# Kernel optimization log

Measured on AMD Instinct MI355X. Metric: run time of the kernel, lower is better.

Reference implementation:

```python
import jax, jax.numpy as jnp
import numpy as np

B, N, D = 256, 128, 512
NUM_TYPES, NUM_STATS = 6, 8
W_TYPE, W_STATS, W_CORR = 1.0, 1.0, 0.5
LN_EPS = 1e-5


def setup_inputs() -> dict:
    key = jax.random.key(0)
    ks = jax.random.split(key, 20)
    s = 1.0 / np.sqrt(D)
    inp = {
        "column_embeddings": jax.random.normal(ks[0], (B, N, D), jnp.float32),
        "masked_columns": jax.random.bernoulli(ks[1], 0.15, (B, N)),
        "type_targets": jax.random.randint(ks[2], (N,), 0, NUM_TYPES),
        "column_statistics": jax.random.normal(ks[3], (B, N, NUM_STATS), jnp.float32),
        "column_correlations": jnp.tanh(jax.random.normal(ks[4], (B, N, N), jnp.float32)),
        # type head: Linear(D,D) -> GELU -> LayerNorm -> Linear(D,NUM_TYPES)
        "t_W1": jax.random.normal(ks[5], (D, D), jnp.float32) * s,
        "t_b1": jnp.zeros((D,), jnp.float32),
        "t_g": jnp.ones((D,), jnp.float32),
        "t_beta": jnp.zeros((D,), jnp.float32),
        "t_W2": jax.random.normal(ks[6], (D, NUM_TYPES), jnp.float32) * s,
        "t_b2": jnp.zeros((NUM_TYPES,), jnp.float32),
        # stats head
        "s_W1": jax.random.normal(ks[7], (D, D), jnp.float32) * s,
        "s_b1": jnp.zeros((D,), jnp.float32),
        "s_g": jnp.ones((D,), jnp.float32),
        "s_beta": jnp.zeros((D,), jnp.float32),
        "s_W2": jax.random.normal(ks[8], (D, NUM_STATS), jnp.float32) * s,
        "s_b2": jnp.zeros((NUM_STATS,), jnp.float32),
        # bilinear correlation: x_i^T W x_j + b
        "c_W": jax.random.normal(ks[9], (D, D), jnp.float32) * s,
        "c_b": jnp.zeros((), jnp.float32),
    }
    return inp


def _mlp_head(x, W1, b1, g, beta, W2, b2):
    h = jax.nn.gelu(x @ W1 + b1, approximate=False)
    mu = h.mean(-1, keepdims=True)
    var = ((h - mu) ** 2).mean(-1, keepdims=True)
    h = (h - mu) * jax.lax.rsqrt(var + LN_EPS) * g + beta
    return h @ W2 + b2


def _forward(column_embeddings, masked_columns, type_targets,
             column_statistics, column_correlations,
             t_W1, t_b1, t_g, t_beta, t_W2, t_b2,
             s_W1, s_b1, s_g, s_beta, s_W2, s_b2,
             c_W, c_b):
    e = column_embeddings  # [B,N,D]
    type_logits = _mlp_head(e, t_W1, t_b1, t_g, t_beta, t_W2, t_b2)   # [B,N,T]
    stats_preds = _mlp_head(e, s_W1, s_b1, s_g, s_beta, s_W2, s_b2)   # [B,N,S]

    # batched bilinear correlation: tanh(e_i W e_j + b), diag forced to 1
    u = jnp.einsum('bnd,de->bne', e, c_W)            # [B,N,D]
    corr = jnp.tanh(jnp.einsum('bne,bme->bnm', u, e) + c_b)  # [B,N,N]
    eye = jnp.eye(e.shape[1], dtype=corr.dtype)
    corr = corr * (1.0 - eye) + eye

    m = masked_columns.astype(jnp.float32)           # [B,N]
    n_masked = jnp.maximum(m.sum(), 1.0)

    # type loss: masked-mean cross entropy; targets broadcast over batch
    logp = jax.nn.log_softmax(type_logits, axis=-1)
    tgt = jnp.broadcast_to(type_targets[None, :], m.shape)
    ce = -jnp.take_along_axis(logp, tgt[..., None], axis=-1)[..., 0]  # [B,N]
    type_loss = (ce * m).sum() / n_masked

    # stats loss: masked-mean MSE over [B,N,S]
    se = (stats_preds - column_statistics) ** 2
    stats_loss = (se * m[..., None]).sum() / (n_masked * se.shape[-1])

    # correlation loss: mask_expanded = m_i | m_j
    me = jnp.maximum(m[:, :, None], m[:, None, :])   # [B,N,N]
    n_me = jnp.maximum(me.sum(), 1.0)
    ce2 = (corr - column_correlations) ** 2
    correlation_loss = (ce2 * me).sum() / n_me

    total = W_TYPE * type_loss + W_STATS * stats_loss + W_CORR * correlation_loss
    return total


def reference(column_embeddings, masked_columns, type_targets,
              column_statistics, column_correlations,
              t_W1, t_b1, t_g, t_beta, t_W2, t_b2,
              s_W1, s_b1, s_g, s_beta, s_W2, s_b2,
              c_W, c_b):
    return _forward(column_embeddings, masked_columns, type_targets,
                    column_statistics, column_correlations,
                    t_W1, t_b1, t_g, t_beta, t_W2, t_b2,
                    s_W1, s_b1, s_g, s_beta, s_W2, s_b2,
                    c_W, c_b)
```

## Files before the change

### kernel.cpp

```cpp
#include <hip/hip_runtime.h>
#include <math.h>

#define Bx 256
#define Nx 128
#define Dx 512
#define NTYPES 6
#define NSTATS 8
#define LN_EPS 1e-5f
#define CAP 8192

typedef __attribute__((ext_vector_type(8))) short frag8;
typedef __attribute__((ext_vector_type(4))) float f32x4;

__device__ __forceinline__ unsigned short f2bf(float f) {
    unsigned u = __float_as_uint(f);
    u += 0x7fff + ((u >> 16) & 1);
    return (unsigned short)(u >> 16);
}
__device__ __forceinline__ float bf2f(unsigned short s) {
    return __uint_as_float((unsigned)s << 16);
}

#define ASYNC16(g, l) __builtin_amdgcn_global_load_lds(                      \
    (const __attribute__((address_space(1))) void*)(g),                      \
    (__attribute__((address_space(3))) void*)(l), 16, 0, 0)

#define VWAIT(NIMM)                                                          \
    asm volatile("s_waitcnt vmcnt(" #NIMM ")" ::: "memory");                 \
    __builtin_amdgcn_sched_barrier(0);
#define BARX __builtin_amdgcn_s_barrier();

#define EB_OFF    0ULL
#define HC_OFF    33554432ULL
#define WT_OFF    67108864ULL
#define WTC_OFF   68157440ULL
#define WC_OFF    68681728ULL
#define LIST_OFF  69206016ULL
#define CNTS_OFF  69238784ULL
#define BASES_OFF 69239808ULL
#define CNTP_OFF  69240832ULL
#define ACC_OFF   69240848ULL
#define DONE_OFF  69240864ULL

__global__ __launch_bounds__(256) void k_prep(
    const float* __restrict__ e, const float* __restrict__ W0,
    const float* __restrict__ W1, const float* __restrict__ W2,
    unsigned short* __restrict__ Eb, unsigned short* __restrict__ Tcmb,
    unsigned short* __restrict__ Tc, unsigned short* __restrict__ Wc,
    const int* __restrict__ m, int* __restrict__ list,
    int* __restrict__ cnts, int* __restrict__ bases, int* cntp) {
    const int bid = blockIdx.x;
    const int t = threadIdx.x;
    if (bid < 256) {
        const int b = bid;
        const int r = b * Nx + t;
        int v = 0;
        if (t < 128) v = (m[r] != 0) ? 1 : 0;
        const unsigned long long bal = __ballot(v);
        const int wid = t >> 6, lane = t & 63;
        __shared__ int wcnt[2];
        __shared__ int base;
        if (lane == 0 && wid < 2) wcnt[wid] = __popcll(bal);
        __syncthreads();
        const int cnt = wcnt[0] + wcnt[1];
        if (t == 0) {
            base = atomicAdd(cntp, cnt);
            cnts[b] = cnt;
            bases[b] = base;
        }
        __syncthreads();
        if (t < 128 && v) {
            const int rank = __popcll(bal & ((1ULL << lane) - 1)) +
                             (wid ? wcnt[0] : 0);
            const int p = base + rank;
            if (p < CAP) list[p] = r;
        }
        return;
    }
    if (bid < 448) {
        const int lin = bid - 256;
        const int mid = lin >> 6;
        const int tl  = lin & 63;
        const int ti = tl >> 3, tj = tl & 7;
        const float* W = (mid == 0) ? W0 : (mid == 1) ? W1 : W2;
        unsigned short* T = (mid == 2) ? Tc : (Tcmb + mid * 262144);
        __shared__ float sh[64][65];
        const int c = t & 63;
        const int r4 = t >> 6;
#pragma unroll
        for (int rr = 0; rr < 16; ++rr) {
            const int row = rr * 4 + r4;
            sh[row][c] = W[(size_t)(ti * 64 + row) * Dx + tj * 64 + c];
        }
        __syncthreads();
#pragma unroll
        for (int rr = 0; rr < 16; ++rr) {
            const int col2 = rr * 4 + r4;
            T[(size_t)(tj * 64 + col2) * Dx + ti * 64 + c] = f2bf(sh[c][col2]);
        }
        return;
    }
    if (bid < 512) {
        const int base = (bid - 448) * 4096 + t * 16;
        const float4* src = (const float4*)(W2 + base);
        unsigned short o[16];
#pragma unroll
        for (int q = 0; q < 4; ++q) {
            const float4 v = src[q];
            o[q * 4 + 0] = f2bf(v.x); o[q * 4 + 1] = f2bf(v.y);
            o[q * 4 + 2] = f2bf(v.z); o[q * 4 + 3] = f2bf(v.w);
        }
        *(uint4*)(Wc + base) = *(const uint4*)(o);
        *(uint4*)(Wc + base + 8) = *(const uint4*)(o + 8);
        return;
    }
    const int r = (bid - 512) * 4 + (t >> 6);
    const int lane = t & 63;
    const float4* src = (const float4*)(e + (size_t)r * Dx);
    const float4 a = src[lane * 2];
    const float4 b = src[lane * 2 + 1];
    unsigned short u[8] = {f2bf(a.x), f2bf(a.y), f2bf(a.z), f2bf(a.w),
                           f2bf(b.x), f2bf(b.y), f2bf(b.z), f2bf(b.w)};
    ((uint4*)(Eb + (size_t)r * Dx))[lane] = *(const uint4*)u;
}

__global__ __launch_bounds__(512) void k_gemms(
    const unsigned short* __restrict__ Eb,
    const unsigned short* __restrict__ Wtcmb,
    const unsigned short* __restrict__ Wtc,
    const unsigned short* __restrict__ Wc,
    const float* __restrict__ bias0, const float* __restrict__ bias1,
    unsigned short* __restrict__ Hc,
    const int* __restrict__ list, const int* __restrict__ cntp) {
    __shared__ unsigned short As[2 * 4096];
    __shared__ unsigned short Bs[2 * 8192];
    const int bid = blockIdx.x;
    const int t = threadIdx.x;
    const int cnt = min(*cntp, CAP);
    const int rt = ((bid >> 6) << 3) | (bid & 7);
    const int row0 = rt << 7;
    if (row0 >= cnt) return;
    const int ct = (bid >> 3) & 7;
    const int col0 = ct << 8;
    const unsigned short* Bbase =
        (ct < 4) ? (Wtcmb + (size_t)ct * 256 * Dx)
      : (ct < 6) ? (Wtc + (size_t)(ct - 4) * 256 * Dx)
                 : (Wc + (size_t)(ct - 6) * 256 * Dx);
    const int kq = (t & 3) ^ ((t >> 3) & 3);
    const int ra = list[min(row0 + (t >> 2), cnt - 1)];
    const unsigned short* pA = Eb + (size_t)ra * Dx + kq * 8;
    const unsigned short* pB0 = Bbase + (size_t)(t >> 2) * Dx + kq * 8;
    const unsigned short* pB1 = pB0 + (size_t)128 * Dx;
    const int w = t >> 6, l = t & 63;
    const int wr = (w >> 2) * 64, wcol = (w & 3) * 64;
    const int quad = l >> 4, mr = l & 15;
    const int co = (quad ^ ((mr >> 1) & 3)) * 8;

#define MSTAGE(bf, k0)                                                       \
  { ASYNC16(pA + (k0), As + (bf) * 4096 + t * 8);                            \
    ASYNC16(pB0 + (k0), Bs + (bf) * 8192 + t * 8);                           \
    ASYNC16(pB1 + (k0), Bs + (bf) * 8192 + 4096 + t * 8); }

    f32x4 acc[4][4] = {};
    MSTAGE(0, 0);
    int buf = 0;
    for (int k = 0; k < 16; ++k) {
        if (k < 15) { MSTAGE(buf ^ 1, (k + 1) * 32); VWAIT(3); }
        else        { VWAIT(0); }
        BARX;
        frag8 af[4], bfv[4];
#pragma unroll
        for (int i = 0; i < 4; ++i)
            af[i] = *(const frag8*)&As[buf * 4096 + (wr + i * 16 + mr) * 32 + co];
#pragma unroll
        for (int j = 0; j < 4; ++j)
            bfv[j] = *(const frag8*)&Bs[buf * 8192 + (wcol + j * 16 + mr) * 32 + co];
        __builtin_amdgcn_s_setprio(1);
#pragma unroll
        for (int i = 0; i < 4; ++i)
#pragma unroll
            for (int j = 0; j < 4; ++j)
                acc[i][j] = __builtin_amdgcn_mfma_f32_16x16x32_bf16(
                    af[i], bfv[j], acc[i][j], 0, 0, 0);
        __builtin_amdgcn_s_setprio(0);
        if (k < 15) BARX;
        buf ^= 1;
    }
#pragma unroll
    for (int i = 0; i < 4; ++i)
#pragma unroll
        for (int j = 0; j < 4; ++j)
#pragma unroll
            for (int r = 0; r < 4; ++r) {
                const int row = row0 + wr + i * 16 + quad * 4 + r;
                const int col = col0 + wcol + j * 16 + mr;
                float v = acc[i][j][r];
                if (col < 1024) {
                    v += (col < 512) ? bias0[col] : bias1[col - 512];
                    v = 0.5f * v * (1.0f + erff(v * 0.70710678118654752f));
                }
                Hc[(size_t)row * 2048 + col] = f2bf(v);
            }
#undef MSTAGE
}

__global__ __launch_bounds__(256) void k_tail(
    const unsigned short* __restrict__ Eb,
    const float* __restrict__ Ct, const int* __restrict__ m,
    const float* __restrict__ cbp,
    const unsigned short* __restrict__ Hc,
    const float* __restrict__ tg, const float* __restrict__ tbeta,
    const float* __restrict__ tW2, const float* __restrict__ tb2,
    const float* __restrict__ sg, const float* __restrict__ sbeta,
    const float* __restrict__ sW2, const float* __restrict__ sb2,
    const int* __restrict__ list, const int* __restrict__ cnts,
    const int* __restrict__ bases, const int* __restrict__ cntp,
    const int* __restrict__ tgt, const float* __restrict__ stats,
    float* __restrict__ accs, int* __restrict__ done,
    float* __restrict__ out) {
    __shared__ unsigned short Elds[2 * 4096];
    __shared__ unsigned short Ulds[2 * 1024];
    __shared__ unsigned short Vlds[2 * 1024];
    __shared__ float mloc[128];
    __shared__ int lrow[128];
    __shared__ float redf[4][2];
    const int t = threadIdx.x;
    const int w = t >> 6, l = t & 63;
    const int quad = l >> 4, mr = l & 15;

    if (blockIdx.x < 256) {
        const int b = blockIdx.x;
        const int cnt = cnts[b];
        const int cbase = bases[b];
        if (t < 128) {
            mloc[t] = (m[b * Nx + t] != 0) ? 1.0f : 0.0f;
            lrow[t] = (t < cnt) ? (list[cbase + t] & (Nx - 1)) : 0;
        }
        __syncthreads();
        float T1 = 0.0f, T2 = 0.0f, Tov = 0.0f;
        const float cb = cbp[0];
        const float* Ctb = Ct + (size_t)b * Nx * Nx;
        if (cnt > 0) {
            const int kq = (t & 3) ^ ((t >> 3) & 3);
            const size_t rb = (size_t)b * Nx;
            const unsigned short* pE0 = Eb + (rb + (t >> 2)) * Dx + kq * 8;
            const unsigned short* pE1 = Eb + (rb + 64 + (t >> 2)) * Dx + kq * 8;
            const int co = (quad ^ ((mr >> 1) & 3)) * 8;
            const int hw = t >> 7;
            const int t2 = t & 127;

            for (int c0 = 0; c0 < cnt; c0 += 32) {
                const int ntc = min(((cnt - c0) + 15) >> 4, 2);
                const int urow = min(c0 + (t2 >> 2), cnt - 1);
                const unsigned short* pUV = Hc + (size_t)(cbase + urow) * 2048
                                            + (hw ? 1536 : 1024) + kq * 8;
                unsigned short* UVdst = hw ? Vlds : Ulds;

#define TSTAGE(bf, ph)                                                       \
  { ASYNC16(pE0 + (ph) * 32, Elds + (bf) * 4096 + t * 8);                    \
    ASYNC16(pE1 + (ph) * 32, Elds + (bf) * 4096 + 2048 + t * 8);             \
    ASYNC16(pUV + (ph) * 32, UVdst + (bf) * 1024 + t2 * 8); }

                f32x4 ar[2][2] = {};
                f32x4 ac[2][2] = {};
                TSTAGE(0, 0);
                int buf = 0;
                for (int k = 0; k < 16; ++k) {
                    if (k < 15) { TSTAGE(buf ^ 1, k + 1); VWAIT(3); }
                    else        { VWAIT(0); }
                    BARX;
                    frag8 ef[2];
#pragma unroll
                    for (int eidx = 0; eidx < 2; ++eidx)
                        ef[eidx] = *(const frag8*)&Elds[buf * 4096 +
                            (w * 32 + eidx * 16 + mr) * 32 + co];
                    __builtin_amdgcn_s_setprio(1);
#pragma unroll
                    for (int it = 0; it < 2; ++it)
                        if (it < ntc) {
                            const frag8 uf = *(const frag8*)&Ulds[buf * 1024 +
                                (it * 16 + mr) * 32 + co];
                            ar[it][0] = __builtin_amdgcn_mfma_f32_16x16x32_bf16(
                                uf, ef[0], ar[it][0], 0, 0, 0);
                            ar[it][1] = __builtin_amdgcn_mfma_f32_16x16x32_bf16(
                                uf, ef[1], ar[it][1], 0, 0, 0);
                        }
#pragma unroll
                    for (int jt = 0; jt < 2; ++jt)
                        if (jt < ntc) {
                            const frag8 vf = *(const frag8*)&Vlds[buf * 1024 +
                                (jt * 16 + mr) * 32 + co];
                            ac[0][jt] = __builtin_amdgcn_mfma_f32_16x16x32_bf16(
                                ef[0], vf, ac[0][jt], 0, 0, 0);
                            ac[1][jt] = __builtin_amdgcn_mfma_f32_16x16x32_bf16(
                                ef[1], vf, ac[1][jt], 0, 0, 0);
                        }
                    __builtin_amdgcn_s_setprio(0);
                    if (k < 15) BARX;
                    buf ^= 1;
                }
#pragma unroll
                for (int it = 0; it < 2; ++it)
                    if (it < ntc) {
#pragma unroll
                        for (int eidx = 0; eidx < 2; ++eidx) {
                            const int j = w * 32 + eidx * 16 + mr;
#pragma unroll
                            for (int r = 0; r < 4; ++r) {
                                const int pos = c0 + it * 16 + quad * 4 + r;
                                if (pos < cnt) {
                                    const int i = lrow[pos];
                                    const float s = ar[it][eidx][r];
                                    const float c = (i == j) ? 1.0f
                                                             : tanhf(s + cb);
                                    const float d = c - Ctb[i * Nx + j];
                                    T1 += d * d;
                                    Tov += d * d * mloc[j];
                                }
                            }
                        }
                    }
#pragma unroll
                for (int jt = 0; jt < 2; ++jt)
                    if (jt < ntc) {
                        const int pos = c0 + jt * 16 + mr;
                        const int valid = (pos < cnt);
                        const int j = lrow[pos & 127];
#pragma unroll
                        for (int eidx = 0; eidx < 2; ++eidx) {
#pragma unroll
                            for (int r = 0; r < 4; ++r) {
                                if (valid) {
                                    const int i = w * 32 + eidx * 16 +
                                                  quad * 4 + r;
                                    const float s = ac[eidx][jt][r];
                                    const float c = (i == j) ? 1.0f
                                                             : tanhf(s + cb);
                                    const float d = c - Ctb[i * Nx + j];
                                    T2 += d * d;
                                }
                            }
                        }
                    }
#undef TSTAGE
            }
        }
        float lsum = T1 + T2 - Tov;
#pragma unroll
        for (int off = 32; off > 0; off >>= 1) lsum += __shfl_down(lsum, off);
        if (l == 0) redf[w][0] = lsum;
        __syncthreads();
        if (t == 0) {
            atomicAdd(&accs[2], redf[0][0] + redf[1][0] + redf[2][0] + redf[3][0]);
            const float c = (float)cnt;
            atomicAdd(&accs[3], 256.0f * c - c * c);
        }
    } else {
        const int blk = blockIdx.x - 256;
        const int cnt = min(*cntp, CAP);
        float ce_acc = 0.0f, sse_acc = 0.0f;
        for (int idx = blk * 4 + w; idx < cnt; idx += 256 * 4) {
            const int r = list[idx];
            const uint4 ut = ((const uint4*)(Hc + (size_t)idx * 2048))[l];
            const uint4 us = ((const uint4*)(Hc + (size_t)idx * 2048 + 512))[l];
            float a[8], b8[8];
            {
                const unsigned uu[4] = {ut.x, ut.y, ut.z, ut.w};
                const unsigned vv[4] = {us.x, us.y, us.z, us.w};
#pragma unroll
                for (int j = 0; j < 4; ++j) {
                    a[2 * j]      = bf2f((unsigned short)(uu[j] & 0xffff));
                    a[2 * j + 1]  = bf2f((unsigned short)(uu[j] >> 16));
                    b8[2 * j]     = bf2f((unsigned short)(vv[j] & 0xffff));
                    b8[2 * j + 1] = bf2f((unsigned short)(vv[j] >> 16));
                }
            }
            float st = 0, qt = 0, ss = 0, qs = 0;
#pragma unroll
            for (int j = 0; j < 8; ++j) {
                st += a[j]; qt += a[j] * a[j];
                ss += b8[j]; qs += b8[j] * b8[j];
            }
#pragma unroll
            for (int off = 32; off > 0; off >>= 1) {
                st += __shfl_xor(st, off); qt += __shfl_xor(qt, off);
                ss += __shfl_xor(ss, off); qs += __shfl_xor(qs, off);
            }
            const float mt = st * (1.0f / Dx);
            const float rt = rsqrtf(qt * (1.0f / Dx) - mt * mt + LN_EPS);
            const float ms = ss * (1.0f / Dx);
            const float rs = rsqrtf(qs * (1.0f / Dx) - ms * ms + LN_EPS);

            const int c0 = l * 8;
            float tp[6] = {}, sp[8] = {};
#pragma unroll
            for (int j = 0; j < 8; ++j) {
                const int c = c0 + j;
                const float nt2 = (a[j] - mt) * rt * tg[c] + tbeta[c];
#pragma unroll
                for (int k = 0; k < 6; ++k) tp[k] += nt2 * tW2[c * 6 + k];
                const float ns = (b8[j] - ms) * rs * sg[c] + sbeta[c];
#pragma unroll
                for (int k = 0; k < 8; ++k) sp[k] += ns * sW2[c * 8 + k];
            }
#pragma unroll
            for (int k = 0; k < 6; ++k)
#pragma unroll
                for (int off = 32; off > 0; off >>= 1) tp[k] += __shfl_down(tp[k], off);
#pragma unroll
            for (int k = 0; k < 8; ++k)
#pragma unroll
                for (int off = 32; off > 0; off >>= 1) sp[k] += __shfl_down(sp[k], off);

            if (l == 0) {
                float lg[6];
#pragma unroll
                for (int k = 0; k < 6; ++k) lg[k] = tp[k] + tb2[k];
                float mx = lg[0];
#pragma unroll
                for (int k = 1; k < 6; ++k) mx = fmaxf(mx, lg[k]);
                float se = 0.0f;
#pragma unroll
                for (int k = 0; k < 6; ++k) se += expf(lg[k] - mx);
                ce_acc += -(lg[tgt[r & (Nx - 1)]] - mx - logf(se));
                float sse = 0.0f;
#pragma unroll
                for (int k = 0; k < 8; ++k) {
                    const float d = sp[k] + sb2[k] - stats[(size_t)r * NSTATS + k];
                    sse += d * d;
                }
                sse_acc += sse;
            }
        }
        if (l == 0) { redf[w][0] = ce_acc; redf[w][1] = sse_acc; }
        __syncthreads();
        if (t == 0) {
            atomicAdd(&accs[0], redf[0][0] + redf[1][0] + redf[2][0] + redf[3][0]);
            atomicAdd(&accs[1], redf[0][1] + redf[1][1] + redf[2][1] + redf[3][1]);
        }
    }
    __syncthreads();
    if (t == 0) {
        __threadfence();
        const int old = atomicAdd(done, 1);
        if (old == 511) {
            __threadfence();
            const float CE  = atomicAdd(&accs[0], 0.0f);
            const float SSE = atomicAdd(&accs[1], 0.0f);
            const float CO  = atomicAdd(&accs[2], 0.0f);
            const float ME  = atomicAdd(&accs[3], 0.0f);
            const float nm = fmaxf((float)min(*cntp, CAP), 1.0f);
            out[0] = CE / nm + SSE / (nm * (float)NSTATS) +
                     0.5f * CO / fmaxf(ME, 1.0f);
        }
    }
}

extern "C" void kernel_launch(void* const* d_in, const int* in_sizes, int n_in,
                              void* d_out, int out_size, void* d_ws, size_t ws_size,
                              hipStream_t stream) {
    const float* e      = (const float*)d_in[0];
    const int*   mcols  = (const int*)d_in[1];
    const int*   ttgt   = (const int*)d_in[2];
    const float* stats  = (const float*)d_in[3];
    const float* corrT  = (const float*)d_in[4];
    const float* tW1    = (const float*)d_in[5];
    const float* tb1    = (const float*)d_in[6];
    const float* tg     = (const float*)d_in[7];
    const float* tbeta  = (const float*)d_in[8];
    const float* tW2    = (const float*)d_in[9];
    const float* tb2    = (const float*)d_in[10];
    const float* sW1    = (const float*)d_in[11];
    const float* sb1    = (const float*)d_in[12];
    const float* sg     = (const float*)d_in[13];
    const float* sbeta  = (const float*)d_in[14];
    const float* sW2    = (const float*)d_in[15];
    const float* sb2    = (const float*)d_in[16];
    const float* cW     = (const float*)d_in[17];
    const float* cb     = (const float*)d_in[18];
    float* out = (float*)d_out;

    char* ws = (char*)d_ws;
    unsigned short* Eb    = (unsigned short*)(ws + EB_OFF);
    unsigned short* Hc    = (unsigned short*)(ws + HC_OFF);
    unsigned short* Wtcmb = (unsigned short*)(ws + WT_OFF);
    unsigned short* Wtc   = (unsigned short*)(ws + WTC_OFF);
    unsigned short* Wc    = (unsigned short*)(ws + WC_OFF);
    int*   list  = (int*)(ws + LIST_OFF);
    int*   cnts  = (int*)(ws + CNTS_OFF);
    int*   bases = (int*)(ws + BASES_OFF);
    int*   cntp  = (int*)(ws + CNTP_OFF);
    float* accs  = (float*)(ws + ACC_OFF);
    int*   done  = (int*)(ws + DONE_OFF);

    hipMemsetAsync(ws + CNTP_OFF, 0, 48, stream);
    k_prep<<<8704, 256, 0, stream>>>(e, tW1, sW1, cW, Eb, Wtcmb, Wtc, Wc,
                                     mcols, list, cnts, bases, cntp);
    k_gemms<<<512, 512, 0, stream>>>(Eb, Wtcmb, Wtc, Wc, tb1, sb1, Hc,
                                     list, cntp);
    k_tail<<<512, 256, 0, stream>>>(Eb, corrT, mcols, cb, Hc,
                                    tg, tbeta, tW2, tb2, sg, sbeta, sW2, sb2,
                                    list, cnts, bases, cntp, ttgt, stats,
                                    accs, done, out);
}
```

Before: 226.0 us.

## Split correlation tail work into half-batch blocks with triple-buffered async loads

The correlation part of k_tail now launches two blocks per batch, each handling 64 of the 128 columns, so there are 512 correlation blocks instead of 256. That doubles parallelism and halves per-block MFMA and register accumulators. The E/U/V LDS staging moves from a double buffer to a three-stage ring with prefetch two steps ahead, so load latency overlaps with compute. The cost is that each U/V tile is loaded twice (once per half-block), and the mask-count atomic is restricted to one half to avoid double counting.

```diff
diff --git a/kernel.cpp b/kernel.cpp
--- a/kernel.cpp
+++ b/kernel.cpp
@@ -218,9 +218,9 @@
     const int* __restrict__ tgt, const float* __restrict__ stats,
     float* __restrict__ accs, int* __restrict__ done,
     float* __restrict__ out) {
-    __shared__ unsigned short Elds[2 * 4096];
-    __shared__ unsigned short Ulds[2 * 1024];
-    __shared__ unsigned short Vlds[2 * 1024];
+    __shared__ unsigned short Elds[3 * 2048];
+    __shared__ unsigned short Ulds[3 * 1024];
+    __shared__ unsigned short Vlds[3 * 1024];
     __shared__ float mloc[128];
     __shared__ int lrow[128];
     __shared__ float redf[4][2];
@@ -228,8 +228,9 @@
     const int w = t >> 6, l = t & 63;
     const int quad = l >> 4, mr = l & 15;
 
-    if (blockIdx.x < 256) {
-        const int b = blockIdx.x;
+    if (blockIdx.x < 512) {
+        const int b = blockIdx.x >> 1;
+        const int h = blockIdx.x & 1;
         const int cnt = cnts[b];
         const int cbase = bases[b];
         if (t < 128) {
@@ -242,81 +243,69 @@
         const float* Ctb = Ct + (size_t)b * Nx * Nx;
         if (cnt > 0) {
             const int kq = (t & 3) ^ ((t >> 3) & 3);
-            const size_t rb = (size_t)b * Nx;
-            const unsigned short* pE0 = Eb + (rb + (t >> 2)) * Dx + kq * 8;
-            const unsigned short* pE1 = Eb + (rb + 64 + (t >> 2)) * Dx + kq * 8;
-            const int co = (quad ^ ((mr >> 1) & 3)) * 8;
+            const size_t rb = (size_t)b * Nx + h * 64;
+            const unsigned short* pE = Eb + (rb + (t >> 2)) * Dx + kq * 8;
             const int hw = t >> 7;
             const int t2 = t & 127;
+            const int kq2 = (t2 & 3) ^ ((t2 >> 3) & 3);
+            const int co = (quad ^ ((mr >> 1) & 3)) * 8;
 
             for (int c0 = 0; c0 < cnt; c0 += 32) {
                 const int ntc = min(((cnt - c0) + 15) >> 4, 2);
                 const int urow = min(c0 + (t2 >> 2), cnt - 1);
                 const unsigned short* pUV = Hc + (size_t)(cbase + urow) * 2048
-                                            + (hw ? 1536 : 1024) + kq * 8;
+                                            + (hw ? 1536 : 1024) + kq2 * 8;
                 unsigned short* UVdst = hw ? Vlds : Ulds;
 
 #define TSTAGE(bf, ph)                                                       \
-  { ASYNC16(pE0 + (ph) * 32, Elds + (bf) * 4096 + t * 8);                    \
-    ASYNC16(pE1 + (ph) * 32, Elds + (bf) * 4096 + 2048 + t * 8);             \
+  { ASYNC16(pE + (ph) * 32, Elds + (bf) * 2048 + t * 8);                     \
     ASYNC16(pUV + (ph) * 32, UVdst + (bf) * 1024 + t2 * 8); }
 
-                f32x4 ar[2][2] = {};
-                f32x4 ac[2][2] = {};
-                TSTAGE(0, 0);
-                int buf = 0;
+                f32x4 ar[2] = {};
+                f32x4 ac[2] = {};
+                TSTAGE(0, 0); TSTAGE(1, 1);
                 for (int k = 0; k < 16; ++k) {
-                    if (k < 15) { TSTAGE(buf ^ 1, k + 1); VWAIT(3); }
-                    else        { VWAIT(0); }
+                    if (k < 15) { VWAIT(2); } else { VWAIT(0); }
                     BARX;
-                    frag8 ef[2];
-#pragma unroll
-                    for (int eidx = 0; eidx < 2; ++eidx)
-                        ef[eidx] = *(const frag8*)&Elds[buf * 4096 +
-                            (w * 32 + eidx * 16 + mr) * 32 + co];
+                    if (k < 14) TSTAGE((k + 2) % 3, k + 2);
+                    const int buf = k % 3;
+                    const frag8 ef = *(const frag8*)&Elds[buf * 2048 +
+                        (w * 16 + mr) * 32 + co];
                     __builtin_amdgcn_s_setprio(1);
 #pragma unroll
                     for (int it = 0; it < 2; ++it)
                         if (it < ntc) {
                             const frag8 uf = *(const frag8*)&Ulds[buf * 1024 +
                                 (it * 16 + mr) * 32 + co];
-                            ar[it][0] = __builtin_amdgcn_mfma_f32_16x16x32_bf16(
-                                uf, ef[0], ar[it][0], 0, 0, 0);
-                            ar[it][1] = __builtin_amdgcn_mfma_f32_16x16x32_bf16(
-                                uf, ef[1], ar[it][1], 0, 0, 0);
+                            ar[it] = __builtin_amdgcn_mfma_f32_16x16x32_bf16(
+                                uf, ef, ar[it], 0, 0, 0);
                         }
 #pragma unroll
                     for (int jt = 0; jt < 2; ++jt)
                         if (jt < ntc) {
                             const frag8 vf = *(const frag8*)&Vlds[buf * 1024 +
                                 (jt * 16 + mr) * 32 + co];
-                            ac[0][jt] = __builtin_amdgcn_mfma_f32_16x16x32_bf16(
-                                ef[0], vf, ac[0][jt], 0, 0, 0);
-                            ac[1][jt] = __builtin_amdgcn_mfma_f32_16x16x32_bf16(
-                                ef[1], vf, ac[1][jt], 0, 0, 0);
+                            ac[jt] = __builtin_amdgcn_mfma_f32_16x16x32_bf16(
+                                ef, vf, ac[jt], 0, 0, 0);
                         }
                     __builtin_amdgcn_s_setprio(0);
                     if (k < 15) BARX;
-                    buf ^= 1;
                 }
+                const int j1 = h * 64 + w * 16 + mr;
 #pragma unroll
                 for (int it = 0; it < 2; ++it)
                     if (it < ntc) {
 #pragma unroll
-                        for (int eidx = 0; eidx < 2; ++eidx) {
-                            const int j = w * 32 + eidx * 16 + mr;
-#pragma unroll
-                            for (int r = 0; r < 4; ++r) {
-                                const int pos = c0 + it * 16 + quad * 4 + r;
-                                if (pos < cnt) {
-                                    const int i = lrow[pos];
-                                    const float s = ar[it][eidx][r];
-                                    const float c = (i == j) ? 1.0f
-                                                             : tanhf(s + cb);
-                                    const float d = c - Ctb[i * Nx + j];
-                                    T1 += d * d;
-                                    Tov += d * d * mloc[j];
-                                }
+                        for (int r = 0; r < 4; ++r) {
+                            const int pos = c0 + it * 16 + quad * 4 + r;
+                            if (pos < cnt) {
+                                const int i = lrow[pos];
+                                const float s = ar[it][r];
+                                const float c = (i == j1) ? 1.0f
+                                                          : tanhf(s + cb);
+                                const float d = c - Ctb[i * Nx + j1];
+                                T1 += d * d;
+                                Tov += d * d * mloc[j1];
                             }
                         }
                     }
@@ -327,18 +316,14 @@
                         const int valid = (pos < cnt);
                         const int j = lrow[pos & 127];
 #pragma unroll
-                        for (int eidx = 0; eidx < 2; ++eidx) {
-#pragma unroll
-                            for (int r = 0; r < 4; ++r) {
-                                if (valid) {
-                                    const int i = w * 32 + eidx * 16 +
-                                                  quad * 4 + r;
-                                    const float s = ac[eidx][jt][r];
-                                    const float c = (i == j) ? 1.0f
-                                                             : tanhf(s + cb);
-                                    const float d = c - Ctb[i * Nx + j];
-                                    T2 += d * d;
-                                }
+                        for (int r = 0; r < 4; ++r) {
+                            if (valid) {
+                                const int i = h * 64 + w * 16 + quad * 4 + r;
+                                const float s = ac[jt][r];
+                                const float c = (i == j) ? 1.0f
+                                                         : tanhf(s + cb);
+                                const float d = c - Ctb[i * Nx + j];
+                                T2 += d * d;
                             }
                         }
                     }
@@ -352,11 +337,13 @@
         __syncthreads();
         if (t == 0) {
             atomicAdd(&accs[2], redf[0][0] + redf[1][0] + redf[2][0] + redf[3][0]);
-            const float c = (float)cnt;
-            atomicAdd(&accs[3], 256.0f * c - c * c);
+            if (h == 0) {
+                const float c = (float)cnt;
+                atomicAdd(&accs[3], 256.0f * c - c * c);
+            }
         }
     } else {
-        const int blk = blockIdx.x - 256;
+        const int blk = blockIdx.x - 512;
         const int cnt = min(*cntp, CAP);
         float ce_acc = 0.0f, sse_acc = 0.0f;
         for (int idx = blk * 4 + w; idx < cnt; idx += 256 * 4) {
@@ -443,7 +430,7 @@
     if (t == 0) {
         __threadfence();
         const int old = atomicAdd(done, 1);
-        if (old == 511) {
+        if (old == 767) {
             __threadfence();
             const float CE  = atomicAdd(&accs[0], 0.0f);
             const float SSE = atomicAdd(&accs[1], 0.0f);
@@ -498,7 +485,7 @@
                                      mcols, list, cnts, bases, cntp);
     k_gemms<<<512, 512, 0, stream>>>(Eb, Wtcmb, Wtc, Wc, tb1, sb1, Hc,
                                      list, cntp);
-    k_tail<<<512, 256, 0, stream>>>(Eb, corrT, mcols, cb, Hc,
+    k_tail<<<768, 256, 0, stream>>>(Eb, corrT, mcols, cb, Hc,
                                     tg, tbeta, tW2, tb2, sg, sbeta, sW2, sb2,
                                     list, cnts, bases, cntp, ttgt, stats,
                                     accs, done, out);
```

Result: slower. 242.1 us (+7.2%).
